# Kernel optimization log

Measured on AMD Instinct MI355X. Metric: run time of the kernel, lower is better.

## Reference

```python
import jax, jax.numpy as jnp
import numpy as np

K_NB = 16
HID = 64
CIN = 128
EPS = 1e-5


def knn_idx(q, t, k):
    # q [B,N,3] queries, t [B,M,3] targets -> idx [B,N,k] into targets
    d = (jnp.sum(q * q, -1)[:, :, None] + jnp.sum(t * t, -1)[:, None, :]
         - 2.0 * jnp.einsum('bnd,bmd->bnm', q, t))
    _, idx = jax.lax.top_k(-d, k)
    return idx


def gather(feat, idx):
    # feat [B,C,M], idx [B,N,K] -> [B,C,N,K]
    return jax.vmap(lambda f, i: f[:, i])(feat, idx)


def conv1x1(x, W, b):
    # x [B,C,N,K], W [O,C], b [O]
    return jnp.einsum('oc,bcnk->bonk', W, x) + b[None, :, None, None]


def group_norm(x, gamma, beta, groups):
    B, C, N, K = x.shape
    xg = x.reshape(B, groups, C // groups, N, K)
    m = xg.mean(axis=(2, 3, 4), keepdims=True)
    v = xg.var(axis=(2, 3, 4), keepdims=True)
    xg = (xg - m) / jnp.sqrt(v + EPS)
    x = xg.reshape(B, C, N, K)
    return x * gamma[None, :, None, None] + beta[None, :, None, None]


def leaky(x):
    return jnp.where(x >= 0, x, 0.1 * x)


def setup_inputs() -> dict:
    key = jax.random.key(0)
    ks = jax.random.split(key, 20)
    B, N = 2, 4096
    d = {
        'xyz0': jax.random.normal(ks[0], (B, 3, N), jnp.float32),
        'xyz1': jax.random.normal(ks[1], (B, 3, N), jnp.float32),
        'state': jax.random.normal(ks[2], (B, HID, N), jnp.float32),
        'corr0': jax.random.normal(ks[3], (B, HID, N), jnp.float32),
        'feat0': jax.random.normal(ks[4], (B, CIN, N), jnp.float32),
        'feat1': jax.random.normal(ks[5], (B, CIN, N), jnp.float32),
        'flow0': jax.random.normal(ks[6], (B, 3, N), jnp.float32),
        # flow_layer: SetConv(3, [64,64]) -> convs take 3+3=6 then 64 in-chans
        'fw1': jax.random.normal(ks[7], (64, 6), jnp.float32) * 0.05,
        'fb1': jnp.zeros((64,), jnp.float32),
        'fg1': jnp.ones((64,), jnp.float32),
        'fbe1': jnp.zeros((64,), jnp.float32),
        'fw2': jax.random.normal(ks[8], (64, 64), jnp.float32) * 0.05,
        'fb2': jnp.zeros((64,), jnp.float32),
        'fg2': jnp.ones((64,), jnp.float32),
        'fbe2': jnp.zeros((64,), jnp.float32),
        # GRU gates: SetConv in_feat = hid(64)+(hid+64=128)=192, +3 = 195 -> 64, no act
        'wz': jax.random.normal(ks[9], (HID, 195), jnp.float32) * 0.05,
        'bz': jnp.zeros((HID,), jnp.float32),
        'wr': jax.random.normal(ks[10], (HID, 195), jnp.float32) * 0.05,
        'br': jnp.zeros((HID,), jnp.float32),
        'wq': jax.random.normal(ks[11], (HID, 195), jnp.float32) * 0.05,
        'bq': jnp.zeros((HID,), jnp.float32),
        # interp weight_net: 2*128+3=259 -> 128 -> 64
        'wa1': jax.random.normal(ks[12], (CIN, 2 * CIN + 3), jnp.float32) * 0.05,
        'ba1': jnp.zeros((CIN,), jnp.float32),
        'wa2': jax.random.normal(ks[13], (HID, CIN), jnp.float32) * 0.05,
        'ba2': jnp.zeros((HID,), jnp.float32),
    }
    return d


def reference(xyz0, xyz1, state, corr0, feat0, feat1, flow0,
              fw1, fb1, fg1, fbe1, fw2, fb2, fg2, fbe2,
              wz, bz, wr, br, wq, bq, wa1, ba1, wa2, ba2):
    xyz0_t = xyz0.transpose(0, 2, 1)  # [B,N,3]
    xyz1_t = xyz1.transpose(0, 2, 1)

    # ---- flow_layer: SetConv (KNN, N==npoint so new_xyz = xyz0) ----
    idx0 = knn_idx(xyz0_t, xyz0_t, K_NB)              # [B,N,K]
    gxyz0 = gather(xyz0, idx0) - xyz0[:, :, :, None]  # [B,3,N,K]
    h = jnp.concatenate([gather(flow0, idx0), gxyz0], axis=1)  # [B,6,N,K]
    h = leaky(group_norm(conv1x1(h, fw1, fb1), fg1, fbe1, 64 // 16))
    h = leaky(group_norm(conv1x1(h, fw2, fb2), fg2, fbe2, 64 // 16))
    flow_feat = h.max(axis=3)  # [B,64,N]

    # ---- iter_layer: SetGRU over xyz0 neighbors ----
    feat_g = jnp.concatenate([corr0, flow_feat], axis=1)  # [B,128,N]

    def gate(f, W, b):
        g = jnp.concatenate([gather(f, idx0), gxyz0], axis=1)
        return conv1x1(g, W, b).max(axis=3)  # [B,64,N]

    hid_in = jnp.concatenate([feat_g, state], axis=1)  # [B,192,N]
    z = jax.nn.sigmoid(gate(hid_in, wz, bz))
    r = jax.nn.sigmoid(gate(hid_in, wr, br))
    q = jnp.tanh(gate(jnp.concatenate([feat_g, r * state], axis=1), wq, bq))
    next_state = (1.0 - z) * state + z * q  # [B,64,N]

    # ---- align_layer: SetInterp (queries xyz1, targets xyz0) ----
    idx1 = knn_idx(xyz1_t, xyz0_t, K_NB)
    gv = gather(next_state, idx1)                        # [B,64,N,K]
    gx = gather(xyz0, idx1) - xyz1[:, :, :, None]        # [B,3,N,K]
    gf = jnp.concatenate([
        gather(feat0, idx1),
        jnp.broadcast_to(feat1[:, :, :, None], feat1.shape + (K_NB,))], axis=1)
    w = conv1x1(jnp.concatenate([gf, gx], axis=1), wa1, ba1)
    w = conv1x1(leaky(w), wa2, ba2)
    w = jax.nn.softmax(w, axis=3)
    return jnp.sum(gv * w, axis=3)  # [B,64,N]
```

## Files before the change

### kernel.cpp

```cpp
#include <hip/hip_runtime.h>

#define B_SZ 2

__device__ __forceinline__ int rfl(int x) { return __builtin_amdgcn_readfirstlane(x); }
__device__ __forceinline__ float leaky(float v) { return v >= 0.f ? v : 0.1f * v; }

__launch_bounds__(256)
__global__ void pack_kernel(const float* __restrict__ xyz, float4* __restrict__ out, int N)
{
  int b = blockIdx.y;
  int i = blockIdx.x * 256 + threadIdx.x;
  if (i >= N) return;
  const float* p = xyz + (size_t)b * 3 * N;
  float x = p[i], y = p[N + i], z = p[2 * N + i];
  out[(size_t)b * N + i] = make_float4(x, y, z, x * x + y * y + z * z);
}

__device__ __forceinline__ void sort64(float& d, int& i, int lane)
{
#pragma unroll
  for (int k = 2; k <= 64; k <<= 1) {
#pragma unroll
    for (int j = k >> 1; j > 0; j >>= 1) {
      float od = __shfl_xor(d, j, 64);
      int   oi = __shfl_xor(i, j, 64);
      bool mineSmall = (d < od) || (d == od && i < oi);
      bool amLow = (lane & j) == 0;
      bool up = (lane & k) == 0;
      bool keepMine = (amLow == up) ? mineSmall : !mineSmall;
      if (!keepMine) { d = od; i = oi; }
    }
  }
}

__launch_bounds__(256)
__global__ void knn_wave_kernel(const float4* __restrict__ pk, const float* __restrict__ q,
                                int* __restrict__ idx, int N)
{
  __shared__ __align__(16) float4 ts[1024];
  __shared__ uint2 buf[4][256];
  const int b = blockIdx.y;
  const int lane = threadIdx.x & 63, wav = rfl(threadIdx.x >> 6);
  const int qi = blockIdx.x * 4 + wav;
  const float* qb = q + (size_t)b * 3 * N;
  const float qx = qb[qi], qy = qb[N + qi], qz = qb[2 * N + qi];
  const float qq = qx * qx + qy * qy + qz * qz;
  const float4* pb = pk + (size_t)b * N;

  float lmin = 3.0e38f;
  for (int ch = 0; ch < N; ch += 1024) {
    __syncthreads();
    for (int i = threadIdx.x; i < 1024; i += 256) ts[i] = pb[ch + i];
    __syncthreads();
#pragma unroll 4
    for (int sub = 0; sub < 16; ++sub) {
      float4 v = ts[sub * 64 + lane];
      float key = (qq + v.w) - 2.0f * (qx * v.x + qy * v.y + qz * v.z);
      lmin = fminf(lmin, key);
    }
  }
  float gm = fminf(lmin, __shfl_xor(lmin, 1, 64));
  gm = fminf(gm, __shfl_xor(gm, 2, 64));
  float t0 = gm;
  t0 = fmaxf(t0, __shfl_xor(t0, 4, 64));
  t0 = fmaxf(t0, __shfl_xor(t0, 8, 64));
  t0 = fmaxf(t0, __shfl_xor(t0, 16, 64));
  t0 = fmaxf(t0, __shfl_xor(t0, 32, 64));

  int cnt = 0;
  for (int ch = 0; ch < N; ch += 1024) {
    __syncthreads();
    for (int i = threadIdx.x; i < 1024; i += 256) ts[i] = pb[ch + i];
    __syncthreads();
    for (int sub = 0; sub < 16; ++sub) {
      float4 v = ts[sub * 64 + lane];
      float key = (qq + v.w) - 2.0f * (qx * v.x + qy * v.y + qz * v.z);
      bool qf = key <= t0;
      unsigned long long mask = __ballot(qf);
      if (mask) {
        unsigned lo = __builtin_amdgcn_mbcnt_lo((unsigned)mask, 0u);
        unsigned pre = __builtin_amdgcn_mbcnt_hi((unsigned)(mask >> 32), lo);
        if (qf) {
          unsigned slot = (unsigned)cnt + pre;
          if (slot < 256u)
            buf[wav][slot] = make_uint2(__float_as_uint(key), (unsigned)(ch + sub * 64 + lane));
        }
        cnt += (int)__popcll(mask);
      }
    }
  }
  int C = cnt < 256 ? cnt : 256;

  float kd = 3.0e38f; int ki = 0x7fffffff;
  if (lane < C) { uint2 u = buf[wav][lane]; kd = __uint_as_float(u.x); ki = (int)u.y; }
  sort64(kd, ki, lane);
  int consumed = C < 64 ? C : 64;
  while (consumed < C) {
    if (lane >= 16) {
      int j2 = consumed + (lane - 16);
      if (j2 < C) { uint2 u = buf[wav][j2]; kd = __uint_as_float(u.x); ki = (int)u.y; }
      else { kd = 3.0e38f; ki = 0x7fffffff; }
    }
    int t = C - consumed; consumed += (t < 48 ? t : 48);
    sort64(kd, ki, lane);
  }
  if (lane < 16) idx[((size_t)b * N + qi) * 16 + lane] = ki;
}

__launch_bounds__(256)
__global__ void prep_w_kernel(const float* __restrict__ wz, const float* __restrict__ wr,
    const float* __restrict__ wq, const float* __restrict__ wa1,
    const float* __restrict__ bz, const float* __restrict__ br,
    float* __restrict__ WtZR, float* __restrict__ WtQ,
    float* __restrict__ WtU, float* __restrict__ WtV, float* __restrict__ bZR)
{
  int job = blockIdx.x;
  int tid = threadIdx.x;
  if (job == 0) {
    for (int e = tid; e < 195 * 128; e += 256) {
      int k = e >> 7, o = e & 127;
      const float* w = (o < 64) ? wz : wr;
      WtZR[(size_t)k * 128 + o] = w[(size_t)(o & 63) * 195 + k];
    }
    if (tid < 128) bZR[tid] = (tid < 64) ? bz[tid] : br[tid - 64];
  } else if (job == 1) {
    for (int e = tid; e < 195 * 64; e += 256) {
      int k = e >> 6, o = e & 63;
      WtQ[(size_t)k * 64 + o] = wq[(size_t)o * 195 + k];
    }
  } else if (job == 2) {
    for (int e = tid; e < 131 * 128; e += 256) {
      int k = e >> 7, o = e & 127;
      int col = (k < 128) ? k : 256 + (k - 128);
      WtU[(size_t)k * 128 + o] = wa1[(size_t)o * 259 + col];
    }
  } else {
    for (int e = tid; e < 131 * 128; e += 256) {
      int k = e >> 7, o = e & 127;
      float v = (k < 128) ? wa1[(size_t)o * 259 + 128 + k]
                          : -wa1[(size_t)o * 259 + 256 + (k - 128)];
      WtV[(size_t)k * 128 + o] = v;
    }
  }
}

#define KC 66
__launch_bounds__(256)
__global__ void projT_kernel(const float* __restrict__ Wt, int K, int WOUT,
    const float* __restrict__ bias, float* __restrict__ out,
    int N, int PN,
    const float* __restrict__ s0, int c0, int l0,
    const float* __restrict__ s1, int c1, int l1,
    const float* __restrict__ s2, int c2, int l2,
    const float* __restrict__ s3, int c3, int l3)
{
  __shared__ __align__(16) float Ws[KC][68];
  __shared__ __align__(16) float Xs[KC][68];
  const int n0 = blockIdx.x * 64;
  const int oo = blockIdx.y * 64;
  const int b = n0 / N;
  const int nn0 = n0 - b * N;
  const int tid = threadIdx.x;
  const int tx = tid & 15, ty = tid >> 4;
  const int o4 = tx * 4, n4 = ty * 4;
  float acc[4][4];
#pragma unroll
  for (int i = 0; i < 4; ++i)
#pragma unroll
    for (int j = 0; j < 4; ++j)
      acc[i][j] = bias ? bias[oo + o4 + j] : 0.0f;

  const int e01 = c0 + c1, e012 = c0 + c1 + c2;
  for (int k0 = 0; k0 < K; k0 += KC) {
    const int kc = min(KC, K - k0);
    __syncthreads();
    for (int e = tid; e < kc * 64; e += 256) {
      int k = e >> 6, o = e & 63;
      Ws[k][o] = Wt[(size_t)(k0 + k) * WOUT + oo + o];
    }
    for (int e = tid; e < kc * 64; e += 256) {
      int k = e >> 6, j = e & 63;
      int c = k0 + k;
      float v;
      if (c < c0)        v = l0 ? s0[(size_t)c * PN + n0 + j]
                                : s0[((size_t)b * c0 + c) * N + nn0 + j];
      else if (c < e01)  { int cc = c - c0;
                           v = l1 ? s1[(size_t)cc * PN + n0 + j]
                                  : s1[((size_t)b * c1 + cc) * N + nn0 + j]; }
      else if (c < e012) { int cc = c - e01;
                           v = l2 ? s2[(size_t)cc * PN + n0 + j]
                                  : s2[((size_t)b * c2 + cc) * N + nn0 + j]; }
      else               { int cc = c - e012;
                           v = l3 ? s3[(size_t)cc * PN + n0 + j]
                                  : s3[((size_t)b * c3 + cc) * N + nn0 + j]; }
      Xs[k][j] = v;
    }
    __syncthreads();
#pragma unroll 2
    for (int k = 0; k < kc; ++k) {
      float4 wv = *(const float4*)&Ws[k][o4];
      float4 xv = *(const float4*)&Xs[k][n4];
      acc[0][0] = fmaf(xv.x, wv.x, acc[0][0]); acc[0][1] = fmaf(xv.x, wv.y, acc[0][1]);
      acc[0][2] = fmaf(xv.x, wv.z, acc[0][2]); acc[0][3] = fmaf(xv.x, wv.w, acc[0][3]);
      acc[1][0] = fmaf(xv.y, wv.x, acc[1][0]); acc[1][1] = fmaf(xv.y, wv.y, acc[1][1]);
      acc[1][2] = fmaf(xv.y, wv.z, acc[1][2]); acc[1][3] = fmaf(xv.y, wv.w, acc[1][3]);
      acc[2][0] = fmaf(xv.z, wv.x, acc[2][0]); acc[2][1] = fmaf(xv.z, wv.y, acc[2][1]);
      acc[2][2] = fmaf(xv.z, wv.z, acc[2][2]); acc[2][3] = fmaf(xv.z, wv.w, acc[2][3]);
      acc[3][0] = fmaf(xv.w, wv.x, acc[3][0]); acc[3][1] = fmaf(xv.w, wv.y, acc[3][1]);
      acc[3][2] = fmaf(xv.w, wv.z, acc[3][2]); acc[3][3] = fmaf(xv.w, wv.w, acc[3][3]);
    }
  }
#pragma unroll
  for (int i = 0; i < 4; ++i) {
    float4 r = make_float4(acc[i][0], acc[i][1], acc[i][2], acc[i][3]);
    *(float4*)&out[(size_t)(n0 + n4 + i) * WOUT + oo + o4] = r;
  }
}

__device__ __forceinline__ void seg_accumL(const float* __restrict__ p, int cnt,
    const float* __restrict__ WL, int sC, int sN, long n0, float acc[4])
{
#pragma unroll 4
  for (int c = 0; c < cnt; ++c) {
    float w = WL[c];
    const float* pp = p + (size_t)c * sC + (size_t)n0 * sN;
#pragma unroll
    for (int m = 0; m < 4; ++m)
      acc[m] = fmaf(w, pp[(size_t)m * sN], acc[m]);
  }
}

template<int WP>
__launch_bounds__(256)
__global__ void proj_kernel(
    const float* __restrict__ W0, const float* __restrict__ bias,
    float* __restrict__ out, int OUTS, int wld, int N,
    const float* __restrict__ s0, int c0, int w0,
    const float* __restrict__ s1, int c1, int w1)
{
  __shared__ float Wl[64 * WP];
  const int b = blockIdx.y;
  const int lane = threadIdx.x & 63;
  const int wav = rfl(threadIdx.x >> 6);
  for (int r = wav; r < 64; r += 4)
    for (int c = lane; c < c0; c += 64)
      Wl[r * WP + c] = W0[(size_t)r * wld + w0 + c];
  for (int r = wav; r < 64; r += 4)
    for (int c = lane; c < c1; c += 64)
      Wl[r * WP + c0 + c] = W0[(size_t)r * wld + w1 + c];
  __syncthreads();
  const long n0 = ((long)blockIdx.x * 4 + wav) * 4;
  float bv = bias ? bias[lane] : 0.0f;
  float acc[4] = {bv, bv, bv, bv};
  const float* WL = &Wl[lane * WP];
  seg_accumL(s0 + (size_t)b * c0 * N, c0, WL, N, 1, n0, acc);
  seg_accumL(s1 + (size_t)b * c1 * N, c1, WL + c0, N, 1, n0, acc);
#pragma unroll
  for (int m = 0; m < 4; ++m)
    out[((size_t)b * N + n0 + m) * OUTS + lane] = acc[m];
}

__launch_bounds__(256)
__global__ void gn1_stats_kernel(const float* __restrict__ G1, const float* __restrict__ xyz0,
    const float* __restrict__ fw1, const int* __restrict__ idx0,
    float* __restrict__ stats1, int N)
{
  __shared__ float red[4][4][2];
  int b = blockIdx.y;
  int lane = threadIdx.x & 63, wav = rfl(threadIdx.x >> 6);
  float wg0 = fw1[lane * 6 + 3], wg1 = fw1[lane * 6 + 4], wg2 = fw1[lane * 6 + 5];
  const float* xb = xyz0 + (size_t)b * 3 * N;
  float sum = 0.f, sq = 0.f;
  for (int n = blockIdx.x * 4 + wav; n < N; n += gridDim.x * 4) {
    const int* ip = idx0 + ((size_t)b * N + n) * 16;
    float bx = wg0 * xb[n] + wg1 * xb[N + n] + wg2 * xb[2 * N + n];
#pragma unroll
    for (int k = 0; k < 16; ++k) {
      int m = ip[k];
      float y = G1[((size_t)b * N + m) * 64 + lane] - bx;
      sum += y; sq += y * y;
    }
  }
#pragma unroll
  for (int off = 1; off < 16; off <<= 1) {
    sum += __shfl_xor(sum, off, 64);
    sq += __shfl_xor(sq, off, 64);
  }
  int g = lane >> 4;
  if ((lane & 15) == 0) { red[wav][g][0] = sum; red[wav][g][1] = sq; }
  __syncthreads();
  if (threadIdx.x < 8) {
    int gg = threadIdx.x >> 1, s = threadIdx.x & 1;
    float v = red[0][gg][s] + red[1][gg][s] + red[2][gg][s] + red[3][gg][s];
    atomicAdd(&stats1[(b * 4 + gg) * 2 + s], v);
  }
}

__global__ void gn_finalize_kernel(const float* __restrict__ raw, float* __restrict__ mi, float cnt)
{
  int i = threadIdx.x;
  if (i < 8) {
    float s = raw[i * 2], q = raw[i * 2 + 1];
    float m = s / cnt;
    float v = q / cnt - m * m;
    mi[i * 2] = m;
    mi[i * 2 + 1] = rsqrtf(v + 1e-5f);
  }
}

__launch_bounds__(256, 2)
__global__ void conv2_kernel(const float* __restrict__ G1, const float* __restrict__ xyz0,
    const float* __restrict__ fw1, const int* __restrict__ idx0,
    const float* __restrict__ fw2, const float* __restrict__ fb2,
    const float* __restrict__ fg1, const float* __restrict__ fbe1,
    const float* __restrict__ mi1, float* __restrict__ y2max, float* __restrict__ y2min,
    float* __restrict__ stats2, int N)
{
  __shared__ __align__(16) float x2[4][16][64];
  __shared__ float red[4][4][2];
  const int b = blockIdx.y;
  const int lane = threadIdx.x & 63;
  const int wav = rfl(threadIdx.x >> 6);
  float4 w[16];
#pragma unroll
  for (int i = 0; i < 16; ++i) w[i] = *(const float4*)&fw2[lane * 64 + i * 4];
  float wg0 = fw1[lane * 6 + 3], wg1 = fw1[lane * 6 + 4], wg2 = fw1[lane * 6 + 5];
  const int g = lane >> 4;
  float mu1 = mi1[(b * 4 + g) * 2], inv1 = mi1[(b * 4 + g) * 2 + 1];
  float sc1 = fg1[lane] * inv1;
  float sh1 = fbe1[lane] - mu1 * sc1;
  float fb2l = fb2[lane];
  const float* xb = xyz0 + (size_t)b * 3 * N;
  float sum = 0.f, sq = 0.f;
  for (int n = blockIdx.x * 4 + wav; n < N; n += gridDim.x * 4) {
    const int* ip = idx0 + ((size_t)b * N + n) * 16;
    float bx = wg0 * xb[n] + wg1 * xb[N + n] + wg2 * xb[2 * N + n];
#pragma unroll
    for (int k = 0; k < 16; ++k) {
      int m = ip[k];
      float y = G1[((size_t)b * N + m) * 64 + lane] - bx;
      x2[wav][k][lane] = leaky(y * sc1 + sh1);
    }
    float acc[16];
#pragma unroll
    for (int k = 0; k < 16; ++k) acc[k] = fb2l;
#pragma unroll
    for (int c4 = 0; c4 < 16; ++c4) {
      float4 w4 = w[c4];
#pragma unroll
      for (int k = 0; k < 16; ++k) {
        float4 x4 = *(const float4*)&x2[wav][k][c4 * 4];
        acc[k] = fmaf(w4.x, x4.x, acc[k]);
        acc[k] = fmaf(w4.y, x4.y, acc[k]);
        acc[k] = fmaf(w4.z, x4.z, acc[k]);
        acc[k] = fmaf(w4.w, x4.w, acc[k]);
      }
    }
    float mx = -3.0e38f, mn = 3.0e38f;
#pragma unroll
    for (int k = 0; k < 16; ++k) {
      mx = fmaxf(mx, acc[k]); mn = fminf(mn, acc[k]);
      sum += acc[k]; sq += acc[k] * acc[k];
    }
    y2max[((size_t)b * N + n) * 64 + lane] = mx;
    y2min[((size_t)b * N + n) * 64 + lane] = mn;
  }
#pragma unroll
  for (int off = 1; off < 16; off <<= 1) {
    sum += __shfl_xor(sum, off, 64);
    sq += __shfl_xor(sq, off, 64);
  }
  if ((lane & 15) == 0) { red[wav][g][0] = sum; red[wav][g][1] = sq; }
  __syncthreads();
  if (threadIdx.x < 8) {
    int gg = threadIdx.x >> 1, s = threadIdx.x & 1;
    float v = red[0][gg][s] + red[1][gg][s] + red[2][gg][s] + red[3][gg][s];
    atomicAdd(&stats2[(b * 4 + gg) * 2 + s], v);
  }
}

__launch_bounds__(256)
__global__ void flow_feat_kernel(const float* __restrict__ y2max, const float* __restrict__ y2min,
    const float* __restrict__ mi2, const float* __restrict__ fg2, const float* __restrict__ fbe2,
    float* __restrict__ ff_t, int N, int PN)
{
  size_t i = (size_t)blockIdx.x * blockDim.x + threadIdx.x;
  if (i >= (size_t)B_SZ * N * 64) return;
  int c = i & 63;
  size_t pn = i >> 6;
  int b = (int)(pn / N);
  int g = c >> 4;
  float mu = mi2[(b * 4 + g) * 2], inv = mi2[(b * 4 + g) * 2 + 1];
  float sc = fg2[c] * inv;
  float sh = fbe2[c] - mu * sc;
  float y = (sc >= 0.0f) ? y2max[i] : y2min[i];
  ff_t[(size_t)c * PN + pn] = leaky(y * sc + sh);
}

__launch_bounds__(256)
__global__ void gate_zr_kernel(const float* __restrict__ Szr,
    const float* __restrict__ wz, const float* __restrict__ wr,
    const float* __restrict__ xyz0, const float* __restrict__ state,
    const int* __restrict__ idx0,
    float* __restrict__ zo, float* __restrict__ rs_t, int N, int PN)
{
  int b = blockIdx.y;
  int lane = threadIdx.x & 63, wav = rfl(threadIdx.x >> 6);
  float wz0 = wz[lane * 195 + 192], wz1 = wz[lane * 195 + 193], wz2 = wz[lane * 195 + 194];
  float wr0 = wr[lane * 195 + 192], wr1 = wr[lane * 195 + 193], wr2 = wr[lane * 195 + 194];
  const float* xb = xyz0 + (size_t)b * 3 * N;
  for (int n = blockIdx.x * 4 + wav; n < N; n += gridDim.x * 4) {
    const int* ip = idx0 + ((size_t)b * N + n) * 16;
    float u0 = xb[n], u1 = xb[N + n], u2 = xb[2 * N + n];
    float xz = wz0 * u0 + wz1 * u1 + wz2 * u2;
    float xr = wr0 * u0 + wr1 * u1 + wr2 * u2;
    float mz = -3.0e38f, mr = -3.0e38f;
#pragma unroll
    for (int k = 0; k < 16; ++k) {
      size_t mo = ((size_t)b * N + ip[k]) * 128 + lane;
      mz = fmaxf(mz, Szr[mo]);
      mr = fmaxf(mr, Szr[mo + 64]);
    }
    size_t no = ((size_t)b * N + n) * 64 + lane;
    float z = 1.f / (1.f + expf(-(mz - xz)));
    float r = 1.f / (1.f + expf(-(mr - xr)));
    zo[no] = z;
    rs_t[(size_t)lane * PN + (size_t)b * N + n] = r * state[((size_t)b * 64 + lane) * N + n];
  }
}

__launch_bounds__(256)
__global__ void gate_q_ns_kernel(const float* __restrict__ Sq, const float* __restrict__ wq,
    const float* __restrict__ xyz0, const float* __restrict__ zo,
    const float* __restrict__ state, const int* __restrict__ idx0,
    float* __restrict__ ns, int N)
{
  int b = blockIdx.y;
  int lane = threadIdx.x & 63, wav = rfl(threadIdx.x >> 6);
  float wq0 = wq[lane * 195 + 192], wq1 = wq[lane * 195 + 193], wq2 = wq[lane * 195 + 194];
  const float* xb = xyz0 + (size_t)b * 3 * N;
  for (int n = blockIdx.x * 4 + wav; n < N; n += gridDim.x * 4) {
    const int* ip = idx0 + ((size_t)b * N + n) * 16;
    float xq = wq0 * xb[n] + wq1 * xb[N + n] + wq2 * xb[2 * N + n];
    float mq = -3.0e38f;
#pragma unroll
    for (int k = 0; k < 16; ++k)
      mq = fmaxf(mq, Sq[((size_t)b * N + ip[k]) * 64 + lane]);
    size_t no = ((size_t)b * N + n) * 64 + lane;
    float q = tanhf(mq - xq);
    float z = zo[no];
    float st = state[((size_t)b * 64 + lane) * N + n];
    ns[no] = (1.f - z) * st + z * q;
  }
}

__launch_bounds__(256, 2)
__global__ void align_kernel(const float* __restrict__ U, const float* __restrict__ V,
    const float* __restrict__ wa2, const float* __restrict__ ba2,
    const float* __restrict__ ns, const int* __restrict__ idx1,
    float* __restrict__ out, int N)
{
  __shared__ __align__(16) float xk[4][16][128];
  const int b = blockIdx.y;
  const int lane = threadIdx.x & 63;
  const int wav = rfl(threadIdx.x >> 6);
  float4 w[32];
#pragma unroll
  for (int i = 0; i < 32; ++i) w[i] = *(const float4*)&wa2[lane * 128 + i * 4];
  float ba = ba2[lane];
  const int n = blockIdx.x * 4 + wav;
  const int* ip = idx1 + ((size_t)b * N + n) * 16;
  int mk[16];
#pragma unroll
  for (int k = 0; k < 16; ++k) mk[k] = ip[k];
  const float* Vp = V + ((size_t)b * N + n) * 128;
  float v0 = Vp[lane], v1 = Vp[64 + lane];
#pragma unroll
  for (int k = 0; k < 16; ++k) {
    const float* Up = U + ((size_t)b * N + mk[k]) * 128;
    xk[wav][k][lane] = leaky(Up[lane] + v0);
    xk[wav][k][64 + lane] = leaky(Up[64 + lane] + v1);
  }
  float acc[16];
#pragma unroll
  for (int k = 0; k < 16; ++k) acc[k] = ba;
#pragma unroll
  for (int c4 = 0; c4 < 32; ++c4) {
    float4 w4 = w[c4];
#pragma unroll
    for (int k = 0; k < 16; ++k) {
      float4 x4 = *(const float4*)&xk[wav][k][c4 * 4];
      acc[k] = fmaf(w4.x, x4.x, acc[k]);
      acc[k] = fmaf(w4.y, x4.y, acc[k]);
      acc[k] = fmaf(w4.z, x4.z, acc[k]);
      acc[k] = fmaf(w4.w, x4.w, acc[k]);
    }
  }
  float m = acc[0];
#pragma unroll
  for (int k = 1; k < 16; ++k) m = fmaxf(m, acc[k]);
  float s = 0.f;
#pragma unroll
  for (int k = 0; k < 16; ++k) { acc[k] = expf(acc[k] - m); s += acc[k]; }
  float rinv = 1.0f / s;
  float o = 0.f;
#pragma unroll
  for (int k = 0; k < 16; ++k)
    o += acc[k] * rinv * ns[((size_t)b * N + mk[k]) * 64 + lane];
  out[((size_t)b * 64 + lane) * N + n] = o;
}

extern "C" void kernel_launch(void* const* d_in, const int* in_sizes, int n_in,
                              void* d_out, int out_size, void* d_ws, size_t ws_size,
                              hipStream_t stream) {
  (void)n_in; (void)out_size; (void)ws_size;
  const float* xyz0 = (const float*)d_in[0];
  const float* xyz1 = (const float*)d_in[1];
  const float* state = (const float*)d_in[2];
  const float* corr0 = (const float*)d_in[3];
  const float* feat0 = (const float*)d_in[4];
  const float* feat1 = (const float*)d_in[5];
  const float* flow0 = (const float*)d_in[6];
  const float* fw1 = (const float*)d_in[7];
  const float* fb1 = (const float*)d_in[8];
  const float* fg1 = (const float*)d_in[9];
  const float* fbe1 = (const float*)d_in[10];
  const float* fw2 = (const float*)d_in[11];
  const float* fb2 = (const float*)d_in[12];
  const float* fg2 = (const float*)d_in[13];
  const float* fbe2 = (const float*)d_in[14];
  const float* wz = (const float*)d_in[15];
  const float* bz = (const float*)d_in[16];
  const float* wr = (const float*)d_in[17];
  const float* br = (const float*)d_in[18];
  const float* wq = (const float*)d_in[19];
  const float* bq = (const float*)d_in[20];
  const float* wa1 = (const float*)d_in[21];
  const float* ba1 = (const float*)d_in[22];
  const float* wa2 = (const float*)d_in[23];
  const float* ba2 = (const float*)d_in[24];
  float* out = (float*)d_out;

  const int N = in_sizes[0] / (3 * B_SZ);
  const int PN = B_SZ * N;
  char* wsb = (char*)d_ws;
  size_t off = 0;
  auto take = [&](size_t bytes) -> char* {
    char* p = wsb + off;
    off += (bytes + 255) & ~(size_t)255;
    return p;
  };
  float* U    = (float*)take((size_t)PN * 128 * 4);
  float* V    = (float*)take((size_t)PN * 128 * 4);
  float* Szr  = (float*)take((size_t)PN * 128 * 4);
  float4* pk0 = (float4*)take((size_t)PN * 4 * 4);
  int*   idx0 = (int*)  take((size_t)PN * 16 * 4);
  int*   idx1 = (int*)  take((size_t)PN * 16 * 4);
  float* G1   = (float*)take((size_t)PN * 64 * 4);
  float* y2mx = (float*)take((size_t)PN * 64 * 4);
  float* y2mn = (float*)take((size_t)PN * 64 * 4);
  float* ff_t = (float*)take((size_t)PN * 64 * 4);
  float* Sq   = (float*)take((size_t)PN * 64 * 4);
  float* zg   = (float*)take((size_t)PN * 64 * 4);
  float* rs_t = (float*)take((size_t)PN * 64 * 4);
  float* ns   = (float*)take((size_t)PN * 64 * 4);
  float* WtZR = (float*)take(195 * 128 * 4);
  float* WtQ  = (float*)take(195 * 64 * 4);
  float* WtU  = (float*)take(131 * 128 * 4);
  float* WtV  = (float*)take(131 * 128 * 4);
  float* bZR  = (float*)take(128 * 4);
  float* stats = (float*)take(256);
  float* raw1 = stats, *raw2 = stats + 16, *mi1 = stats + 32, *mi2 = stats + 48;

  const float* FN = nullptr;
  const float cntv = 16.0f * N * 16.0f;

  hipMemsetAsync(raw1, 0, 32 * sizeof(float), stream);

  pack_kernel<<<dim3((N + 255) / 256, B_SZ), 256, 0, stream>>>(xyz0, pk0, N);
  prep_w_kernel<<<4, 256, 0, stream>>>(wz, wr, wq, wa1, bz, br, WtZR, WtQ, WtU, WtV, bZR);
  knn_wave_kernel<<<dim3(N / 4, B_SZ), 256, 0, stream>>>(pk0, xyz0, idx0, N);
  knn_wave_kernel<<<dim3(N / 4, B_SZ), 256, 0, stream>>>(pk0, xyz1, idx1, N);

  proj_kernel<7><<<dim3(N / 16, B_SZ), 256, 0, stream>>>(
      fw1, fb1, G1, 64, 6, N, flow0, 3, 0, xyz0, 3, 3);

  gn1_stats_kernel<<<dim3(256, B_SZ), 256, 0, stream>>>(G1, xyz0, fw1, idx0, raw1, N);
  gn_finalize_kernel<<<1, 64, 0, stream>>>(raw1, mi1, cntv);
  conv2_kernel<<<dim3(512, B_SZ), 256, 0, stream>>>(G1, xyz0, fw1, idx0, fw2, fb2, fg1, fbe1,
      mi1, y2mx, y2mn, raw2, N);
  gn_finalize_kernel<<<1, 64, 0, stream>>>(raw2, mi2, cntv);
  flow_feat_kernel<<<dim3((unsigned)((size_t)PN * 64 / 256)), 256, 0, stream>>>(
      y2mx, y2mn, mi2, fg2, fbe2, ff_t, N, PN);

  projT_kernel<<<dim3(PN / 64, 2), 256, 0, stream>>>(WtZR, 195, 128, bZR, Szr, N, PN,
      corr0, 64, 0,  ff_t, 64, 1,  state, 64, 0,  xyz0, 3, 0);

  gate_zr_kernel<<<dim3(256, B_SZ), 256, 0, stream>>>(Szr, wz, wr, xyz0, state, idx0, zg, rs_t, N, PN);

  projT_kernel<<<dim3(PN / 64, 1), 256, 0, stream>>>(WtQ, 195, 64, bq, Sq, N, PN,
      corr0, 64, 0,  ff_t, 64, 1,  rs_t, 64, 1,  xyz0, 3, 0);

  gate_q_ns_kernel<<<dim3(256, B_SZ), 256, 0, stream>>>(Sq, wq, xyz0, zg, state, idx0, ns, N);

  projT_kernel<<<dim3(PN / 64, 2), 256, 0, stream>>>(WtU, 131, 128, FN, U, N, PN,
      feat0, 128, 0,  xyz0, 3, 0,  FN, 0, 0,  FN, 0, 0);
  projT_kernel<<<dim3(PN / 64, 2), 256, 0, stream>>>(WtV, 131, 128, ba1, V, N, PN,
      feat1, 128, 0,  xyz1, 3, 0,  FN, 0, 0,  FN, 0, 0);

  align_kernel<<<dim3(N / 4, B_SZ), 256, 0, stream>>>(U, V, wa2, ba2, ns, idx1, out, N);
}
```

Before: 368.2 us.

## Retile align kernel as shared-memory GEMM, merge U/V projections, inline GN finalize

The align kernel now stages the transposed second-layer weights and the gathered, activated neighbor features in shared memory. It computes the 64x128x64 product with a 4x4 register tile per thread and does the softmax and weighted sum through cross-lane shuffles, replacing the old layout that held 128 weight floats per lane. The two U/V projections are merged into one launch via a z-dimension, and the two gn_finalize launches are removed by computing mean and inverse std inline in the consumers. This cuts launch count and register pressure, at the cost of larger shared-memory use per block and a swizzled layout that adds some complexity.

```diff
diff --git a/kernel.cpp b/kernel.cpp
--- a/kernel.cpp
+++ b/kernel.cpp
@@ -109,10 +109,11 @@
 
 __launch_bounds__(256)
 __global__ void prep_w_kernel(const float* __restrict__ wz, const float* __restrict__ wr,
-    const float* __restrict__ wq, const float* __restrict__ wa1,
+    const float* __restrict__ wq, const float* __restrict__ wa1, const float* __restrict__ wa2,
     const float* __restrict__ bz, const float* __restrict__ br,
     float* __restrict__ WtZR, float* __restrict__ WtQ,
-    float* __restrict__ WtU, float* __restrict__ WtV, float* __restrict__ bZR)
+    float* __restrict__ WtU, float* __restrict__ WtV, float* __restrict__ WtA2,
+    float* __restrict__ bZR)
 {
   int job = blockIdx.x;
   int tid = threadIdx.x;
@@ -134,12 +135,17 @@
       int col = (k < 128) ? k : 256 + (k - 128);
       WtU[(size_t)k * 128 + o] = wa1[(size_t)o * 259 + col];
     }
-  } else {
+  } else if (job == 3) {
     for (int e = tid; e < 131 * 128; e += 256) {
       int k = e >> 7, o = e & 127;
       float v = (k < 128) ? wa1[(size_t)o * 259 + 128 + k]
                           : -wa1[(size_t)o * 259 + 256 + (k - 128)];
       WtV[(size_t)k * 128 + o] = v;
+    }
+  } else {
+    for (int e = tid; e < 128 * 64; e += 256) {
+      int c = e >> 6, o = e & 63;
+      WtA2[e] = wa2[(size_t)o * 128 + c];
     }
   }
 }
@@ -193,6 +199,73 @@
       else               { int cc = c - e012;
                            v = l3 ? s3[(size_t)cc * PN + n0 + j]
                                   : s3[((size_t)b * c3 + cc) * N + nn0 + j]; }
+      Xs[k][j] = v;
+    }
+    __syncthreads();
+#pragma unroll 2
+    for (int k = 0; k < kc; ++k) {
+      float4 wv = *(const float4*)&Ws[k][o4];
+      float4 xv = *(const float4*)&Xs[k][n4];
+      acc[0][0] = fmaf(xv.x, wv.x, acc[0][0]); acc[0][1] = fmaf(xv.x, wv.y, acc[0][1]);
+      acc[0][2] = fmaf(xv.x, wv.z, acc[0][2]); acc[0][3] = fmaf(xv.x, wv.w, acc[0][3]);
+      acc[1][0] = fmaf(xv.y, wv.x, acc[1][0]); acc[1][1] = fmaf(xv.y, wv.y, acc[1][1]);
+      acc[1][2] = fmaf(xv.y, wv.z, acc[1][2]); acc[1][3] = fmaf(xv.y, wv.w, acc[1][3]);
+      acc[2][0] = fmaf(xv.z, wv.x, acc[2][0]); acc[2][1] = fmaf(xv.z, wv.y, acc[2][1]);
+      acc[2][2] = fmaf(xv.z, wv.z, acc[2][2]); acc[2][3] = fmaf(xv.z, wv.w, acc[2][3]);
+      acc[3][0] = fmaf(xv.w, wv.x, acc[3][0]); acc[3][1] = fmaf(xv.w, wv.y, acc[3][1]);
+      acc[3][2] = fmaf(xv.w, wv.z, acc[3][2]); acc[3][3] = fmaf(xv.w, wv.w, acc[3][3]);
+    }
+  }
+#pragma unroll
+  for (int i = 0; i < 4; ++i) {
+    float4 r = make_float4(acc[i][0], acc[i][1], acc[i][2], acc[i][3]);
+    *(float4*)&out[(size_t)(n0 + n4 + i) * WOUT + oo + o4] = r;
+  }
+}
+
+__launch_bounds__(256)
+__global__ void projUV_kernel(const float* __restrict__ WtU, const float* __restrict__ WtV,
+    const float* __restrict__ ba1, float* __restrict__ Uo, float* __restrict__ Vo,
+    int N, int PN,
+    const float* __restrict__ feat0, const float* __restrict__ feat1,
+    const float* __restrict__ x0, const float* __restrict__ x1)
+{
+  __shared__ __align__(16) float Ws[KC][68];
+  __shared__ __align__(16) float Xs[KC][68];
+  const int z = blockIdx.z;
+  const float* Wt = z ? WtV : WtU;
+  const float* bias = z ? ba1 : 0;
+  float* out = z ? Vo : Uo;
+  const float* s0 = z ? feat1 : feat0;
+  const float* s1 = z ? x1 : x0;
+  const int K = 131, WOUT = 128, c0 = 128;
+  const int n0 = blockIdx.x * 64;
+  const int oo = blockIdx.y * 64;
+  const int b = n0 / N;
+  const int nn0 = n0 - b * N;
+  const int tid = threadIdx.x;
+  const int tx = tid & 15, ty = tid >> 4;
+  const int o4 = tx * 4, n4 = ty * 4;
+  float acc[4][4];
+#pragma unroll
+  for (int i = 0; i < 4; ++i)
+#pragma unroll
+    for (int j = 0; j < 4; ++j)
+      acc[i][j] = bias ? bias[oo + o4 + j] : 0.0f;
+
+  for (int k0 = 0; k0 < K; k0 += KC) {
+    const int kc = min(KC, K - k0);
+    __syncthreads();
+    for (int e = tid; e < kc * 64; e += 256) {
+      int k = e >> 6, o = e & 63;
+      Ws[k][o] = Wt[(size_t)(k0 + k) * WOUT + oo + o];
+    }
+    for (int e = tid; e < kc * 64; e += 256) {
+      int k = e >> 6, j = e & 63;
+      int c = k0 + k;
+      float v;
+      if (c < c0) v = s0[((size_t)b * c0 + c) * N + nn0 + j];
+      else        v = s1[((size_t)b * 3 + (c - c0)) * N + nn0 + j];
       Xs[k][j] = v;
     }
     __syncthreads();
@@ -296,24 +369,13 @@
   }
 }
 
-__global__ void gn_finalize_kernel(const float* __restrict__ raw, float* __restrict__ mi, float cnt)
-{
-  int i = threadIdx.x;
-  if (i < 8) {
-    float s = raw[i * 2], q = raw[i * 2 + 1];
-    float m = s / cnt;
-    float v = q / cnt - m * m;
-    mi[i * 2] = m;
-    mi[i * 2 + 1] = rsqrtf(v + 1e-5f);
-  }
-}
-
 __launch_bounds__(256, 2)
 __global__ void conv2_kernel(const float* __restrict__ G1, const float* __restrict__ xyz0,
     const float* __restrict__ fw1, const int* __restrict__ idx0,
     const float* __restrict__ fw2, const float* __restrict__ fb2,
     const float* __restrict__ fg1, const float* __restrict__ fbe1,
-    const float* __restrict__ mi1, float* __restrict__ y2max, float* __restrict__ y2min,
+    const float* __restrict__ raw1, float cnt,
+    float* __restrict__ y2max, float* __restrict__ y2min,
     float* __restrict__ stats2, int N)
 {
   __shared__ __align__(16) float x2[4][16][64];
@@ -326,7 +388,9 @@
   for (int i = 0; i < 16; ++i) w[i] = *(const float4*)&fw2[lane * 64 + i * 4];
   float wg0 = fw1[lane * 6 + 3], wg1 = fw1[lane * 6 + 4], wg2 = fw1[lane * 6 + 5];
   const int g = lane >> 4;
-  float mu1 = mi1[(b * 4 + g) * 2], inv1 = mi1[(b * 4 + g) * 2 + 1];
+  float s_ = raw1[(b * 4 + g) * 2], q_ = raw1[(b * 4 + g) * 2 + 1];
+  float mu1 = s_ / cnt;
+  float inv1 = rsqrtf(q_ / cnt - mu1 * mu1 + 1e-5f);
   float sc1 = fg1[lane] * inv1;
   float sh1 = fbe1[lane] - mu1 * sc1;
   float fb2l = fb2[lane];
@@ -381,7 +445,8 @@
 
 __launch_bounds__(256)
 __global__ void flow_feat_kernel(const float* __restrict__ y2max, const float* __restrict__ y2min,
-    const float* __restrict__ mi2, const float* __restrict__ fg2, const float* __restrict__ fbe2,
+    const float* __restrict__ raw2, float cnt,
+    const float* __restrict__ fg2, const float* __restrict__ fbe2,
     float* __restrict__ ff_t, int N, int PN)
 {
   size_t i = (size_t)blockIdx.x * blockDim.x + threadIdx.x;
@@ -390,7 +455,9 @@
   size_t pn = i >> 6;
   int b = (int)(pn / N);
   int g = c >> 4;
-  float mu = mi2[(b * 4 + g) * 2], inv = mi2[(b * 4 + g) * 2 + 1];
+  float s_ = raw2[(b * 4 + g) * 2], q_ = raw2[(b * 4 + g) * 2 + 1];
+  float mu = s_ / cnt;
+  float inv = rsqrtf(q_ / cnt - mu * mu + 1e-5f);
   float sc = fg2[c] * inv;
   float sh = fbe2[c] - mu * sc;
   float y = (sc >= 0.0f) ? y2max[i] : y2min[i];
@@ -456,58 +523,120 @@
 
 __launch_bounds__(256, 2)
 __global__ void align_kernel(const float* __restrict__ U, const float* __restrict__ V,
-    const float* __restrict__ wa2, const float* __restrict__ ba2,
+    const float* __restrict__ WtA2, const float* __restrict__ ba2,
     const float* __restrict__ ns, const int* __restrict__ idx1,
     float* __restrict__ out, int N)
 {
-  __shared__ __align__(16) float xk[4][16][128];
+  __shared__ __align__(16) float Xs[64][128];
+  __shared__ __align__(16) float Ws[128][64];
   const int b = blockIdx.y;
-  const int lane = threadIdx.x & 63;
-  const int wav = rfl(threadIdx.x >> 6);
-  float4 w[32];
-#pragma unroll
-  for (int i = 0; i < 32; ++i) w[i] = *(const float4*)&wa2[lane * 128 + i * 4];
-  float ba = ba2[lane];
+  const int tid = threadIdx.x;
+  const int lane = tid & 63;
+  const int wav = rfl(tid >> 6);
+
+  for (int e = tid; e < 2048; e += 256) {
+    int c = e >> 4, o4 = (e & 15) << 2;
+    *(float4*)&Ws[c][o4] = *(const float4*)&WtA2[(c << 6) + o4];
+  }
+
   const int n = blockIdx.x * 4 + wav;
-  const int* ip = idx1 + ((size_t)b * N + n) * 16;
-  int mk[16];
-#pragma unroll
-  for (int k = 0; k < 16; ++k) mk[k] = ip[k];
-  const float* Vp = V + ((size_t)b * N + n) * 128;
-  float v0 = Vp[lane], v1 = Vp[64 + lane];
-#pragma unroll
-  for (int k = 0; k < 16; ++k) {
-    const float* Up = U + ((size_t)b * N + mk[k]) * 128;
-    xk[wav][k][lane] = leaky(Up[lane] + v0);
-    xk[wav][k][64 + lane] = leaky(Up[64 + lane] + v1);
-  }
-  float acc[16];
-#pragma unroll
-  for (int k = 0; k < 16; ++k) acc[k] = ba;
-#pragma unroll
+  int mkreg = 0;
+  {
+    const int* ip = idx1 + ((size_t)b * N + n) * 16;
+    if (lane < 16) mkreg = ip[lane];
+  }
+  const int c4l = lane & 31;
+  const int half = lane >> 5;
+  float4 v4 = *(const float4*)&V[(((size_t)b * N + n) << 7) + (c4l << 2)];
+  for (int k0 = 0; k0 < 16; k0 += 2) {
+    int k = k0 + half;
+    int m = __shfl(mkreg, k);
+    float4 u4 = *(const float4*)&U[(((size_t)b * N + m) << 7) + (c4l << 2)];
+    float4 xv;
+    xv.x = leaky(u4.x + v4.x);
+    xv.y = leaky(u4.y + v4.y);
+    xv.z = leaky(u4.z + v4.z);
+    xv.w = leaky(u4.w + v4.w);
+    int row = (wav << 4) + k;
+    *(float4*)&Xs[row][(c4l ^ (row & 7)) << 2] = xv;
+  }
+  __syncthreads();
+
+  const int tx = tid & 15, ty = tid >> 4;
+  const int o4 = tx << 2, r0 = ty << 2;
+  float4 bav = *(const float4*)&ba2[o4];
+  float acc[4][4];
+#pragma unroll
+  for (int i = 0; i < 4; ++i) {
+    acc[i][0] = bav.x; acc[i][1] = bav.y; acc[i][2] = bav.z; acc[i][3] = bav.w;
+  }
   for (int c4 = 0; c4 < 32; ++c4) {
-    float4 w4 = w[c4];
-#pragma unroll
-    for (int k = 0; k < 16; ++k) {
-      float4 x4 = *(const float4*)&xk[wav][k][c4 * 4];
-      acc[k] = fmaf(w4.x, x4.x, acc[k]);
-      acc[k] = fmaf(w4.y, x4.y, acc[k]);
-      acc[k] = fmaf(w4.z, x4.z, acc[k]);
-      acc[k] = fmaf(w4.w, x4.w, acc[k]);
-    }
-  }
-  float m = acc[0];
-#pragma unroll
-  for (int k = 1; k < 16; ++k) m = fmaxf(m, acc[k]);
-  float s = 0.f;
-#pragma unroll
-  for (int k = 0; k < 16; ++k) { acc[k] = expf(acc[k] - m); s += acc[k]; }
-  float rinv = 1.0f / s;
-  float o = 0.f;
-#pragma unroll
-  for (int k = 0; k < 16; ++k)
-    o += acc[k] * rinv * ns[((size_t)b * N + mk[k]) * 64 + lane];
-  out[((size_t)b * 64 + lane) * N + n] = o;
+    float4 wv0 = *(const float4*)&Ws[c4 * 4 + 0][o4];
+    float4 wv1 = *(const float4*)&Ws[c4 * 4 + 1][o4];
+    float4 wv2 = *(const float4*)&Ws[c4 * 4 + 2][o4];
+    float4 wv3 = *(const float4*)&Ws[c4 * 4 + 3][o4];
+#pragma unroll
+    for (int i = 0; i < 4; ++i) {
+      int row = r0 + i;
+      float4 xv = *(const float4*)&Xs[row][(c4 ^ (row & 7)) << 2];
+      acc[i][0] = fmaf(xv.x, wv0.x, acc[i][0]);
+      acc[i][1] = fmaf(xv.x, wv0.y, acc[i][1]);
+      acc[i][2] = fmaf(xv.x, wv0.z, acc[i][2]);
+      acc[i][3] = fmaf(xv.x, wv0.w, acc[i][3]);
+      acc[i][0] = fmaf(xv.y, wv1.x, acc[i][0]);
+      acc[i][1] = fmaf(xv.y, wv1.y, acc[i][1]);
+      acc[i][2] = fmaf(xv.y, wv1.z, acc[i][2]);
+      acc[i][3] = fmaf(xv.y, wv1.w, acc[i][3]);
+      acc[i][0] = fmaf(xv.z, wv2.x, acc[i][0]);
+      acc[i][1] = fmaf(xv.z, wv2.y, acc[i][1]);
+      acc[i][2] = fmaf(xv.z, wv2.z, acc[i][2]);
+      acc[i][3] = fmaf(xv.z, wv2.w, acc[i][3]);
+      acc[i][0] = fmaf(xv.w, wv3.x, acc[i][0]);
+      acc[i][1] = fmaf(xv.w, wv3.y, acc[i][1]);
+      acc[i][2] = fmaf(xv.w, wv3.z, acc[i][2]);
+      acc[i][3] = fmaf(xv.w, wv3.w, acc[i][3]);
+    }
+  }
+
+  float m_[4];
+#pragma unroll
+  for (int j = 0; j < 4; ++j) {
+    float m = fmaxf(fmaxf(acc[0][j], acc[1][j]), fmaxf(acc[2][j], acc[3][j]));
+    m = fmaxf(m, __shfl_xor(m, 16, 64));
+    m = fmaxf(m, __shfl_xor(m, 32, 64));
+    m_[j] = m;
+  }
+  float e_[4][4], s_[4];
+#pragma unroll
+  for (int j = 0; j < 4; ++j) {
+    float s = 0.f;
+#pragma unroll
+    for (int i = 0; i < 4; ++i) { e_[i][j] = expf(acc[i][j] - m_[j]); s += e_[i][j]; }
+    s += __shfl_xor(s, 16, 64);
+    s += __shfl_xor(s, 32, 64);
+    s_[j] = s;
+  }
+  float o_[4] = {0.f, 0.f, 0.f, 0.f};
+#pragma unroll
+  for (int i = 0; i < 4; ++i) {
+    int k = (r0 + i) & 15;
+    int m = __shfl(mkreg, k);
+    float4 nsv = *(const float4*)&ns[(((size_t)b * N + m) << 6) + o4];
+    o_[0] = fmaf(e_[i][0], nsv.x, o_[0]);
+    o_[1] = fmaf(e_[i][1], nsv.y, o_[1]);
+    o_[2] = fmaf(e_[i][2], nsv.z, o_[2]);
+    o_[3] = fmaf(e_[i][3], nsv.w, o_[3]);
+  }
+#pragma unroll
+  for (int j = 0; j < 4; ++j) {
+    o_[j] += __shfl_xor(o_[j], 16, 64);
+    o_[j] += __shfl_xor(o_[j], 32, 64);
+  }
+  if ((lane >> 4) == 0) {
+#pragma unroll
+    for (int j = 0; j < 4; ++j)
+      out[((size_t)b * 64 + o4 + j) * N + n] = o_[j] / s_[j];
+  }
 }
 
 extern "C" void kernel_launch(void* const* d_in, const int* in_sizes, int n_in,
@@ -568,17 +697,18 @@
   float* WtQ  = (float*)take(195 * 64 * 4);
   float* WtU  = (float*)take(131 * 128 * 4);
   float* WtV  = (float*)take(131 * 128 * 4);
+  float* WtA2 = (float*)take(128 * 64 * 4);
   float* bZR  = (float*)take(128 * 4);
   float* stats = (float*)take(256);
-  float* raw1 = stats, *raw2 = stats + 16, *mi1 = stats + 32, *mi2 = stats + 48;
-
-  const float* FN = nullptr;
+  float* raw1 = stats, *raw2 = stats + 16;
+
   const float cntv = 16.0f * N * 16.0f;
 
   hipMemsetAsync(raw1, 0, 32 * sizeof(float), stream);
 
   pack_kernel<<<dim3((N + 255) / 256, B_SZ), 256, 0, stream>>>(xyz0, pk0, N);
-  prep_w_kernel<<<4, 256, 0, stream>>>(wz, wr, wq, wa1, bz, br, WtZR, WtQ, WtU, WtV, bZR);
+  prep_w_kernel<<<5, 256, 0, stream>>>(wz, wr, wq, wa1, wa2, bz, br,
+      WtZR, WtQ, WtU, WtV, WtA2, bZR);
   knn_wave_kernel<<<dim3(N / 4, B_SZ), 256, 0, stream>>>(pk0, xyz0, idx0, N);
   knn_wave_kernel<<<dim3(N / 4, B_SZ), 256, 0, stream>>>(pk0, xyz1, idx1, N);
 
@@ -586,12 +716,10 @@
       fw1, fb1, G1, 64, 6, N, flow0, 3, 0, xyz0, 3, 3);
 
   gn1_stats_kernel<<<dim3(256, B_SZ), 256, 0, stream>>>(G1, xyz0, fw1, idx0, raw1, N);
-  gn_finalize_kernel<<<1, 64, 0, stream>>>(raw1, mi1, cntv);
   conv2_kernel<<<dim3(512, B_SZ), 256, 0, stream>>>(G1, xyz0, fw1, idx0, fw2, fb2, fg1, fbe1,
-      mi1, y2mx, y2mn, raw2, N);
-  gn_finalize_kernel<<<1, 64, 0, stream>>>(raw2, mi2, cntv);
+      raw1, cntv, y2mx, y2mn, raw2, N);
   flow_feat_kernel<<<dim3((unsigned)((size_t)PN * 64 / 256)), 256, 0, stream>>>(
-      y2mx, y2mn, mi2, fg2, fbe2, ff_t, N, PN);
+      y2mx, y2mn, raw2, cntv, fg2, fbe2, ff_t, N, PN);
 
   projT_kernel<<<dim3(PN / 64, 2), 256, 0, stream>>>(WtZR, 195, 128, bZR, Szr, N, PN,
       corr0, 64, 0,  ff_t, 64, 1,  state, 64, 0,  xyz0, 3, 0);
@@ -603,10 +731,8 @@
 
   gate_q_ns_kernel<<<dim3(256, B_SZ), 256, 0, stream>>>(Sq, wq, xyz0, zg, state, idx0, ns, N);
 
-  projT_kernel<<<dim3(PN / 64, 2), 256, 0, stream>>>(WtU, 131, 128, FN, U, N, PN,
-      feat0, 128, 0,  xyz0, 3, 0,  FN, 0, 0,  FN, 0, 0);
-  projT_kernel<<<dim3(PN / 64, 2), 256, 0, stream>>>(WtV, 131, 128, ba1, V, N, PN,
-      feat1, 128, 0,  xyz1, 3, 0,  FN, 0, 0,  FN, 0, 0);
-
-  align_kernel<<<dim3(N / 4, B_SZ), 256, 0, stream>>>(U, V, wa2, ba2, ns, idx1, out, N);
-}
+  projUV_kernel<<<dim3(PN / 64, 2, 2), 256, 0, stream>>>(WtU, WtV, ba1, U, V, N, PN,
+      feat0, feat1, xyz0, xyz1);
+
+  align_kernel<<<dim3(N / 4, B_SZ), 256, 0, stream>>>(U, V, WtA2, ba2, ns, idx1, out, N);
+}
```

Result: faster. 337.8 us (-8.3%).
